# Optimization experiments

Hardware: AMD Instinct MI355X
Metric: run time of the kernel (lower is better)

## Reference

```python
import jax, jax.numpy as jnp
import numpy as np
from jax import lax

K = 3
PAD = 1
K2 = K * K


def _conv(x, w, b):
    dn = lax.conv_dimension_numbers(x.shape, w.shape, ('NCHW', 'OIHW', 'NCHW'))
    y = lax.conv_general_dilated(x, w, (1, 1), [(PAD, PAD), (PAD, PAD)], dimension_numbers=dn)
    return y + b[None, :, None, None]


def _gather(x, iy, ix):
    # x: [B,C,H,W]; iy,ix: [B,K2,H,W] int32 -> [B,C,K2,H,W]
    B, C, H, W = x.shape
    flat = x.reshape(B, C, H * W)
    idx = iy * W + ix  # [B,K2,H,W]
    return jax.vmap(lambda xb, ib: xb[:, ib])(flat, idx)


def _deform_conv2d(x, offset_w, offset_b, mask_w, mask_b, weight):
    B, C, H, W = x.shape
    O = weight.shape[0]
    offset = _conv(x, offset_w, offset_b)            # [B,2*K2,H,W]
    mask = jax.nn.sigmoid(_conv(x, mask_w, mask_b))  # [B,K2,H,W]

    off = offset.reshape(B, K2, 2, H, W)
    oy, ox = off[:, :, 0], off[:, :, 1]              # [B,K2,H,W]

    ki = (jnp.arange(K2) // K).astype(x.dtype)       # kernel row per tap
    kj = (jnp.arange(K2) % K).astype(x.dtype)        # kernel col per tap
    base_y = (jnp.arange(H) - PAD).astype(x.dtype)
    base_x = (jnp.arange(W) - PAD).astype(x.dtype)

    py = oy + base_y[None, None, :, None] + ki[None, :, None, None]  # [B,K2,H,W]
    px = ox + base_x[None, None, None, :] + kj[None, :, None, None]

    y0 = jnp.floor(py)
    x0 = jnp.floor(px)
    dy = py - y0
    dx = px - x0
    y0i = y0.astype(jnp.int32)
    x0i = x0.astype(jnp.int32)

    acc = jnp.zeros((B, C, K2, H, W), dtype=x.dtype)
    for (yc, xc, wgt) in [
        (y0i,     x0i,     (1 - dy) * (1 - dx)),
        (y0i,     x0i + 1, (1 - dy) * dx),
        (y0i + 1, x0i,     dy * (1 - dx)),
        (y0i + 1, x0i + 1, dy * dx),
    ]:
        valid = ((yc >= 0) & (yc < H) & (xc >= 0) & (xc < W)).astype(x.dtype)
        g = _gather(x, jnp.clip(yc, 0, H - 1), jnp.clip(xc, 0, W - 1))  # [B,C,K2,H,W]
        acc = acc + g * (wgt * valid)[:, None]

    modulated = acc * mask[:, None]                  # [B,C,K2,H,W]
    w2 = weight.reshape(O, C, K2)
    return jnp.einsum('bckhw,ock->bohw', modulated, w2)


def setup_inputs() -> dict:
    key = jax.random.key(0)
    ks = jax.random.split(key, 6)
    B, C, O, H, W = 4, 64, 64, 128, 128
    return {
        'x': jax.random.normal(ks[0], (B, C, H, W), jnp.float32),
        'offset_w': jax.random.normal(ks[1], (2 * K2, C, K, K), jnp.float32) * 0.05,
        'offset_b': jax.random.normal(ks[2], (2 * K2,), jnp.float32) * 0.05,
        'mask_w': jax.random.normal(ks[3], (K2, C, K, K), jnp.float32) * 0.05,
        'mask_b': jnp.full((K2,), 0.5, jnp.float32),
        'weight': jax.random.normal(ks[5], (O, C, K, K), jnp.float32) * (1.0 / np.sqrt(C * K2)),
    }


def reference(x, offset_w, offset_b, mask_w, mask_b, weight):
    return _deform_conv2d(x, offset_w, offset_b, mask_w, mask_b, weight)
```

## Files before the change

kernel.cpp:

```cpp
#include <hip/hip_runtime.h>
#include <math.h>

#define BB 4
#define CC 64
#define OO 64
#define HH 128
#define WW 128
#define HWsz (HH * WW)

typedef __attribute__((ext_vector_type(8))) _Float16 half8;
typedef __attribute__((ext_vector_type(4))) float floatx4;

__global__ __launch_bounds__(256) void pre_kernel(
    const float* __restrict__ x, const float* __restrict__ wgt,
    const float* __restrict__ ow, const float* __restrict__ mw,
    _Float16* __restrict__ xh, _Float16* __restrict__ waf,
    _Float16* __restrict__ wcf)
{
    int bid = blockIdx.x;
    int tid = threadIdx.x;
    if (bid < 512) {
        int b = bid >> 7, y = bid & 127;
        int px = tid & 127;
        int ch = (tid >> 7) * 32;
        const float* xp = x + (size_t)(b * CC + ch) * HWsz + y * WW + px;
        _Float16 buf[32];
#pragma unroll
        for (int q = 0; q < 32; ++q)
            buf[q] = (_Float16)xp[(size_t)q * HWsz];
        _Float16* dst = xh + ((size_t)(b * HH + y) * WW + px) * 64 + ch;
#pragma unroll
        for (int q = 0; q < 4; ++q)
            *(half8*)&dst[q * 8] = *(const half8*)&buf[q * 8];
    } else {
        int i = (bid - 512) * 256 + tid;
        if (i < 36864) {
            int j = i & 7, lane = (i >> 3) & 63, rest = i >> 9;
            int m = rest & 3, kh = (rest >> 2) & 1, k = rest >> 3;
            int o = m * 16 + (lane & 15);
            int c = kh * 32 + ((lane >> 4) << 3) + j;
            waf[i] = (_Float16)wgt[o * 576 + c * 9 + k];
        } else if (i < 55296) {
            int t = i - 36864;
            int j = t & 7, lane = (t >> 3) & 63, rest = t >> 9;
            int m = rest & 1, kh = (rest >> 1) & 1, k = rest >> 2;
            int o = m * 16 + (lane & 15);
            int c = kh * 32 + ((lane >> 4) << 3) + j;
            float v = 0.f;
            if (o < 18) v = ow[o * 576 + c * 9 + k];
            else if (o < 27) v = mw[(o - 18) * 576 + c * 9 + k];
            wcf[t] = (_Float16)v;
        }
    }
}

__global__ __launch_bounds__(1024, 1) void fused_kernel(
    const _Float16* __restrict__ xh, const _Float16* __restrict__ waf,
    const _Float16* __restrict__ wcf, const float* __restrict__ ob,
    const float* __restrict__ mb, float* __restrict__ out)
{
    __shared__ __align__(16) _Float16 lds_waf[36864];
    __shared__ _Float16 omh[16 * 27 * 16];
    __shared__ __align__(16) _Float16 blendb[16 * 2048];

    int tid = threadIdx.x;
    int gid = blockIdx.x;
    int sid = (gid & 7) * 32 + (gid >> 3);
    int b = sid >> 6;
    int t = sid & 63;
    int rq = t >> 1;
    int q = t & 1;

    int wv = tid >> 6;
    int lane = tid & 63;
    int s = wv & 3;
    int h = rq * 4 + (wv >> 2);
    int p0 = q << 6;
    int g = lane >> 4;
    int pl = lane & 15;
    int goff = g * 8;
    int xw = p0 + s * 16 + pl;
    int oct = lane & 7;
    int pxg = lane >> 3;

    const _Float16* xhb = xh + ((size_t)b << 20);
    _Float16* omw = &omh[wv * 27 * 16];
    _Float16* bbw = &blendb[wv * 2048];

    half8 stg[9];
    if (wv < 8) {
#pragma unroll
        for (int i = 0; i < 9; ++i)
            stg[i] = *(const half8*)(waf + ((wv * 9 + i) << 9) + lane * 8);
    }

    floatx4 accC0 = {0.f, 0.f, 0.f, 0.f};
    floatx4 accC1 = {0.f, 0.f, 0.f, 0.f};

#define CADDR(K, P, V) do {                                                  \
    int ky = (K) / 3, kx = (K) - ky * 3;                                     \
    int yy = h + ky - 1, xx = xw + kx - 1;                                   \
    V = (yy >= 0) & (yy < HH) & (xx >= 0) & (xx < WW);                       \
    int yc = min(max(yy, 0), HH - 1), xc = min(max(xx, 0), WW - 1);          \
    P = ((yc * WW + xc) << 6) + goff;                                        \
} while (0)

#define CONVTAP(K, S0, S1, V) do {                                           \
    const _Float16* wp = wcf + ((K) << 11) + lane * 8;                       \
    half8 w00 = *(const half8*)(wp + (0 << 9));                              \
    half8 w01 = *(const half8*)(wp + (1 << 9));                              \
    half8 w10 = *(const half8*)(wp + (2 << 9));                              \
    half8 w11 = *(const half8*)(wp + (3 << 9));                              \
    half8 z = {0, 0, 0, 0, 0, 0, 0, 0};                                     \
    half8 a0 = (V) ? S0 : z;                                                 \
    half8 a1 = (V) ? S1 : z;                                                 \
    accC0 = __builtin_amdgcn_mfma_f32_16x16x32_f16(w00, a0, accC0, 0, 0, 0); \
    accC1 = __builtin_amdgcn_mfma_f32_16x16x32_f16(w01, a0, accC1, 0, 0, 0); \
    accC0 = __builtin_amdgcn_mfma_f32_16x16x32_f16(w10, a1, accC0, 0, 0, 0); \
    accC1 = __builtin_amdgcn_mfma_f32_16x16x32_f16(w11, a1, accC1, 0, 0, 0); \
} while (0)

    {
        bool vA, vB;
        int pa, pb;
        half8 A0, A1, B0, B1;
        CADDR(0, pa, vA);
        A0 = *(const half8*)(xhb + pa);
        A1 = *(const half8*)(xhb + pa + 32);
#pragma unroll 1
        for (int kp = 0; kp < 4; ++kp) {
            int k = kp * 2;
            CADDR(k + 1, pb, vB);
            B0 = *(const half8*)(xhb + pb);
            B1 = *(const half8*)(xhb + pb + 32);
            CONVTAP(k, A0, A1, vA);
            CADDR(k + 2, pa, vA);
            A0 = *(const half8*)(xhb + pa);
            A1 = *(const half8*)(xhb + pa + 32);
            CONVTAP(k + 1, B0, B1, vB);
        }
        CONVTAP(8, A0, A1, vA);
    }

#pragma unroll
    for (int j = 0; j < 4; ++j) {
        int o = g * 4 + j;
        omw[o * 16 + pl] = (_Float16)(accC0[j] + ob[o]);
        int o2 = 16 + g * 4 + j;
        float v = accC1[j];
        if (o2 < 18) omw[o2 * 16 + pl] = (_Float16)(v + ob[o2]);
        else if (o2 < 27)
            omw[o2 * 16 + pl] =
                (_Float16)(1.0f / (1.0f + expf(-(v + mb[o2 - 18]))));
    }

    if (wv < 8) {
#pragma unroll
        for (int i = 0; i < 9; ++i)
            *(half8*)&lds_waf[((wv * 9 + i) << 9) + lane * 8] = stg[i];
    }
    __syncthreads();

    floatx4 acc0 = {0.f, 0.f, 0.f, 0.f}, acc1 = {0.f, 0.f, 0.f, 0.f};
    floatx4 acc2 = {0.f, 0.f, 0.f, 0.f}, acc3 = {0.f, 0.f, 0.f, 0.f};

#define MKT(K, P, U00, U01, U10, U11, I00, I01, I10, I11) do {               \
    int ky = (K) / 3, kx = (K) - ky * 3;                                     \
    float oy = (float)omw[(2 * (K)) * 16 + (P)];                             \
    float ox = (float)omw[(2 * (K) + 1) * 16 + (P)];                         \
    float mk = (float)omw[(18 + (K)) * 16 + (P)];                            \
    float py = oy + (float)(h + ky - 1);                                     \
    float qx = ox + (float)(p0 + s * 16 + (P) + kx - 1);                     \
    float y0f = floorf(py), x0f = floorf(qx);                                \
    float dyy = py - y0f, dxx = qx - x0f;                                    \
    int y0 = (int)y0f, x0 = (int)x0f;                                        \
    int y1 = y0 + 1, x1 = x0 + 1;                                            \
    bool vy0 = (y0 >= 0) & (y0 < HH), vy1 = (y1 >= 0) & (y1 < HH);           \
    bool vx0 = (x0 >= 0) & (x0 < WW), vx1 = (x1 >= 0) & (x1 < WW);           \
    U00 = (vy0 & vx0) ? (1.f - dyy) * (1.f - dxx) * mk : 0.f;                \
    U01 = (vy0 & vx1) ? (1.f - dyy) * dxx * mk : 0.f;                        \
    U10 = (vy1 & vx0) ? dyy * (1.f - dxx) * mk : 0.f;                        \
    U11 = (vy1 & vx1) ? dyy * dxx * mk : 0.f;                                \
    int yc0 = min(max(y0, 0), HH - 1), yc1 = min(max(y1, 0), HH - 1);        \
    int xc0 = min(max(x0, 0), WW - 1), xc1 = min(max(x1, 0), WW - 1);        \
    I00 = ((yc0 * WW + xc0) << 6) + oct * 8;                                 \
    I01 = ((yc0 * WW + xc1) << 6) + oct * 8;                                 \
    I10 = ((yc1 * WW + xc0) << 6) + oct * 8;                                 \
    I11 = ((yc1 * WW + xc1) << 6) + oct * 8;                                 \
} while (0)

#define SPLAT8(H) ((half8){(H), (H), (H), (H), (H), (H), (H), (H)})
#define MF(Q, B, A) A = __builtin_amdgcn_mfma_f32_16x16x32_f16(Q, B, A, 0, 0, 0)

#define DECLG(S)                                                             \
    float u0##S, u1##S, u2##S, u3##S, u4##S, u5##S, u6##S, u7##S;            \
    half8 r0##S, r1##S, r2##S, r3##S, r4##S, r5##S, r6##S, r7##S;

#define GLOAD(K, S) do {                                                     \
    int i0, i1, i2, i3, i4, i5, i6, i7;                                      \
    MKT(K, pxg, u0##S, u1##S, u2##S, u3##S, i0, i1, i2, i3);                 \
    MKT(K, 8 + pxg, u4##S, u5##S, u6##S, u7##S, i4, i5, i6, i7);             \
    r0##S = *(const half8*)(xhb + i0);                                       \
    r1##S = *(const half8*)(xhb + i1);                                       \
    r2##S = *(const half8*)(xhb + i2);                                       \
    r3##S = *(const half8*)(xhb + i3);                                       \
    r4##S = *(const half8*)(xhb + i4);                                       \
    r5##S = *(const half8*)(xhb + i5);                                       \
    r6##S = *(const half8*)(xhb + i6);                                       \
    r7##S = *(const half8*)(xhb + i7);                                       \
} while (0)

#define BW(K, S) do {                                                        \
    half8 bfA = r0##S * SPLAT8((_Float16)u0##S);                             \
    bfA = bfA + r1##S * SPLAT8((_Float16)u1##S);                             \
    bfA = bfA + r2##S * SPLAT8((_Float16)u2##S);                             \
    bfA = bfA + r3##S * SPLAT8((_Float16)u3##S);                             \
    half8 bfB = r4##S * SPLAT8((_Float16)u4##S);                             \
    bfB = bfB + r5##S * SPLAT8((_Float16)u5##S);                             \
    bfB = bfB + r6##S * SPLAT8((_Float16)u6##S);                             \
    bfB = bfB + r7##S * SPLAT8((_Float16)u7##S);                             \
    _Float16* bb = bbw + (((K) & 1) << 10);                                  \
    *(half8*)&bb[(pxg << 6) + ((oct ^ pxg) << 3)] = bfA;                     \
    *(half8*)&bb[((8 + pxg) << 6) + ((oct ^ pxg) << 3)] = bfB;               \
} while (0)

#define CONS(K) do {                                                         \
    const _Float16* bbr = bbw + (((K) & 1) << 10);                           \
    half8 bf = *(const half8*)&bbr[(pl << 6) + ((g ^ (pl & 7)) << 3)];       \
    half8 bd = *(const half8*)&bbr[(pl << 6) + (((g + 4) ^ (pl & 7)) << 3)]; \
    const _Float16* wk = &lds_waf[((K) << 12) + lane * 8];                   \
    half8 q0 = *(const half8*)(wk + (0 << 9));                               \
    half8 q1 = *(const half8*)(wk + (1 << 9));                               \
    half8 q2 = *(const half8*)(wk + (2 << 9));                               \
    half8 q3 = *(const half8*)(wk + (3 << 9));                               \
    half8 q4 = *(const half8*)(wk + (4 << 9));                               \
    half8 q5 = *(const half8*)(wk + (5 << 9));                               \
    half8 q6 = *(const half8*)(wk + (6 << 9));                               \
    half8 q7 = *(const half8*)(wk + (7 << 9));                               \
    MF(q0, bf, acc0); MF(q1, bf, acc1); MF(q2, bf, acc2); MF(q3, bf, acc3);  \
    MF(q4, bd, acc0); MF(q5, bd, acc1); MF(q6, bd, acc2); MF(q7, bd, acc3);  \
} while (0)

#define ITER(K, S) do {                                                      \
    const _Float16* bbr = bbw + (((K) & 1) << 10);                           \
    half8 bf = *(const half8*)&bbr[(pl << 6) + ((g ^ (pl & 7)) << 3)];       \
    half8 bd = *(const half8*)&bbr[(pl << 6) + (((g + 4) ^ (pl & 7)) << 3)]; \
    GLOAD((K) + 1, S);                                                       \
    const _Float16* wk = &lds_waf[((K) << 12) + lane * 8];                   \
    half8 q0 = *(const half8*)(wk + (0 << 9));                               \
    half8 q1 = *(const half8*)(wk + (1 << 9));                               \
    half8 q2 = *(const half8*)(wk + (2 << 9));                               \
    half8 q3 = *(const half8*)(wk + (3 << 9));                               \
    half8 q4 = *(const half8*)(wk + (4 << 9));                               \
    half8 q5 = *(const half8*)(wk + (5 << 9));                               \
    half8 q6 = *(const half8*)(wk + (6 << 9));                               \
    half8 q7 = *(const half8*)(wk + (7 << 9));                               \
    MF(q0, bf, acc0); MF(q1, bf, acc1); MF(q2, bf, acc2); MF(q3, bf, acc3);  \
    MF(q4, bd, acc0); MF(q5, bd, acc1); MF(q6, bd, acc2); MF(q7, bd, acc3);  \
    BW((K) + 1, S);                                                          \
} while (0)

    {
        DECLG(A)
        DECLG(B)
        GLOAD(0, A);
        BW(0, A);
        ITER(0, B);
        ITER(1, A);
        ITER(2, B);
        ITER(3, A);
        ITER(4, B);
        ITER(5, A);
        ITER(6, B);
        ITER(7, A);
        CONS(8);
    }

    float* outp = out + (size_t)b * OO * HWsz + h * WW + p0 + s * 16 + pl;
#pragma unroll
    for (int j = 0; j < 4; ++j) outp[(size_t)(g * 4 + j) * HWsz] = acc0[j];
#pragma unroll
    for (int j = 0; j < 4; ++j) outp[(size_t)(16 + g * 4 + j) * HWsz] = acc1[j];
#pragma unroll
    for (int j = 0; j < 4; ++j) outp[(size_t)(32 + g * 4 + j) * HWsz] = acc2[j];
#pragma unroll
    for (int j = 0; j < 4; ++j) outp[(size_t)(48 + g * 4 + j) * HWsz] = acc3[j];
}

extern "C" void kernel_launch(void* const* d_in, const int* in_sizes, int n_in,
                              void* d_out, int out_size, void* d_ws, size_t ws_size,
                              hipStream_t stream)
{
    const float* x   = (const float*)d_in[0];
    const float* ow  = (const float*)d_in[1];
    const float* ob  = (const float*)d_in[2];
    const float* mw  = (const float*)d_in[3];
    const float* mb  = (const float*)d_in[4];
    const float* wgt = (const float*)d_in[5];
    float* out = (float*)d_out;

    _Float16* xh  = (_Float16*)d_ws;
    _Float16* waf = xh + (size_t)BB * HWsz * 64;
    _Float16* wcf = waf + 36864;

    pre_kernel<<<dim3(512 + 216), dim3(256), 0, stream>>>(
        x, wgt, ow, mw, xh, waf, wcf);
    fused_kernel<<<dim3(256), dim3(1024), 0, stream>>>(
        xh, waf, wcf, ob, mb, out);
}
```

Before: 44.33 us.

## Stage input halo window in LDS for offset conv; read main weights from global

Each block now cooperatively loads a 6x68 halo window of the fp16 channels-last input into swizzled LDS, and the offset/mask conv taps read from it instead of doing per-wave global loads with bounds checks. To free LDS for the window, the 72KB main-weight staging is removed and the deformable-conv MFMA loop reads its weight fragments directly from global memory (L1/L2 cached). This trades redundant global input reads for an extra barrier and global weight loads in the hot inner loop.

```diff
diff --git a/kernel.cpp b/kernel.cpp
--- a/kernel.cpp
+++ b/kernel.cpp
@@ -59,7 +59,7 @@
     const _Float16* __restrict__ wcf, const float* __restrict__ ob,
     const float* __restrict__ mb, float* __restrict__ out)
 {
-    __shared__ __align__(16) _Float16 lds_waf[36864];
+    __shared__ __align__(16) _Float16 win[6 * 68 * 64];
     __shared__ _Float16 omh[16 * 27 * 16];
     __shared__ __align__(16) _Float16 blendb[16 * 2048];
 
@@ -78,69 +78,58 @@
     int p0 = q << 6;
     int g = lane >> 4;
     int pl = lane & 15;
-    int goff = g * 8;
-    int xw = p0 + s * 16 + pl;
     int oct = lane & 7;
     int pxg = lane >> 3;
+    int h0 = rq * 4;
 
     const _Float16* xhb = xh + ((size_t)b << 20);
     _Float16* omw = &omh[wv * 27 * 16];
     _Float16* bbw = &blendb[wv * 2048];
 
-    half8 stg[9];
-    if (wv < 8) {
-#pragma unroll
-        for (int i = 0; i < 9; ++i)
-            stg[i] = *(const half8*)(waf + ((wv * 9 + i) << 9) + lane * 8);
-    }
+    {
+        half8 z = {0, 0, 0, 0, 0, 0, 0, 0};
+#pragma unroll
+        for (int it = 0; it < 4; ++it) {
+            int ch = tid + it * 1024;
+            if (ch < 3264) {
+                int o8 = ch & 7;
+                int rc = ch >> 3;
+                int r = rc / 68;
+                int cc = rc - r * 68;
+                int gy = h0 - 1 + r;
+                int gx = p0 - 1 + cc;
+                half8 v = z;
+                if ((cc < 66) & (gy >= 0) & (gy < HH) & (gx >= 0) & (gx < WW))
+                    v = *(const half8*)(xhb + (((size_t)gy * WW + gx) << 6) + o8 * 8);
+                *(half8*)&win[((r * 68 + cc) << 6) + ((o8 ^ (cc & 7)) << 3)] = v;
+            }
+        }
+    }
+    __syncthreads();
 
     floatx4 accC0 = {0.f, 0.f, 0.f, 0.f};
     floatx4 accC1 = {0.f, 0.f, 0.f, 0.f};
 
-#define CADDR(K, P, V) do {                                                  \
+#define CONVTAP(K) do {                                                      \
     int ky = (K) / 3, kx = (K) - ky * 3;                                     \
-    int yy = h + ky - 1, xx = xw + kx - 1;                                   \
-    V = (yy >= 0) & (yy < HH) & (xx >= 0) & (xx < WW);                       \
-    int yc = min(max(yy, 0), HH - 1), xc = min(max(xx, 0), WW - 1);          \
-    P = ((yc * WW + xc) << 6) + goff;                                        \
-} while (0)
-
-#define CONVTAP(K, S0, S1, V) do {                                           \
+    int r = (wv >> 2) + ky;                                                  \
+    int c = s * 16 + pl + kx;                                                \
+    const _Float16* wb = &win[((r * 68 + c) << 6)];                          \
+    half8 a0 = *(const half8*)&wb[((g ^ (c & 7)) << 3)];                     \
+    half8 a1 = *(const half8*)&wb[(((g + 4) ^ (c & 7)) << 3)];               \
     const _Float16* wp = wcf + ((K) << 11) + lane * 8;                       \
     half8 w00 = *(const half8*)(wp + (0 << 9));                              \
     half8 w01 = *(const half8*)(wp + (1 << 9));                              \
     half8 w10 = *(const half8*)(wp + (2 << 9));                              \
     half8 w11 = *(const half8*)(wp + (3 << 9));                              \
-    half8 z = {0, 0, 0, 0, 0, 0, 0, 0};                                     \
-    half8 a0 = (V) ? S0 : z;                                                 \
-    half8 a1 = (V) ? S1 : z;                                                 \
     accC0 = __builtin_amdgcn_mfma_f32_16x16x32_f16(w00, a0, accC0, 0, 0, 0); \
     accC1 = __builtin_amdgcn_mfma_f32_16x16x32_f16(w01, a0, accC1, 0, 0, 0); \
     accC0 = __builtin_amdgcn_mfma_f32_16x16x32_f16(w10, a1, accC0, 0, 0, 0); \
     accC1 = __builtin_amdgcn_mfma_f32_16x16x32_f16(w11, a1, accC1, 0, 0, 0); \
 } while (0)
 
-    {
-        bool vA, vB;
-        int pa, pb;
-        half8 A0, A1, B0, B1;
-        CADDR(0, pa, vA);
-        A0 = *(const half8*)(xhb + pa);
-        A1 = *(const half8*)(xhb + pa + 32);
-#pragma unroll 1
-        for (int kp = 0; kp < 4; ++kp) {
-            int k = kp * 2;
-            CADDR(k + 1, pb, vB);
-            B0 = *(const half8*)(xhb + pb);
-            B1 = *(const half8*)(xhb + pb + 32);
-            CONVTAP(k, A0, A1, vA);
-            CADDR(k + 2, pa, vA);
-            A0 = *(const half8*)(xhb + pa);
-            A1 = *(const half8*)(xhb + pa + 32);
-            CONVTAP(k + 1, B0, B1, vB);
-        }
-        CONVTAP(8, A0, A1, vA);
-    }
+    CONVTAP(0); CONVTAP(1); CONVTAP(2); CONVTAP(3); CONVTAP(4);
+    CONVTAP(5); CONVTAP(6); CONVTAP(7); CONVTAP(8);
 
 #pragma unroll
     for (int j = 0; j < 4; ++j) {
@@ -153,13 +142,6 @@
             omw[o2 * 16 + pl] =
                 (_Float16)(1.0f / (1.0f + expf(-(v + mb[o2 - 18]))));
     }
-
-    if (wv < 8) {
-#pragma unroll
-        for (int i = 0; i < 9; ++i)
-            *(half8*)&lds_waf[((wv * 9 + i) << 9) + lane * 8] = stg[i];
-    }
-    __syncthreads();
 
     floatx4 acc0 = {0.f, 0.f, 0.f, 0.f}, acc1 = {0.f, 0.f, 0.f, 0.f};
     floatx4 acc2 = {0.f, 0.f, 0.f, 0.f}, acc3 = {0.f, 0.f, 0.f, 0.f};
@@ -228,7 +210,7 @@
     const _Float16* bbr = bbw + (((K) & 1) << 10);                           \
     half8 bf = *(const half8*)&bbr[(pl << 6) + ((g ^ (pl & 7)) << 3)];       \
     half8 bd = *(const half8*)&bbr[(pl << 6) + (((g + 4) ^ (pl & 7)) << 3)]; \
-    const _Float16* wk = &lds_waf[((K) << 12) + lane * 8];                   \
+    const _Float16* wk = waf + ((K) << 12) + lane * 8;                       \
     half8 q0 = *(const half8*)(wk + (0 << 9));                               \
     half8 q1 = *(const half8*)(wk + (1 << 9));                               \
     half8 q2 = *(const half8*)(wk + (2 << 9));                               \
@@ -246,7 +228,7 @@
     half8 bf = *(const half8*)&bbr[(pl << 6) + ((g ^ (pl & 7)) << 3)];       \
     half8 bd = *(const half8*)&bbr[(pl << 6) + (((g + 4) ^ (pl & 7)) << 3)]; \
     GLOAD((K) + 1, S);                                                       \
-    const _Float16* wk = &lds_waf[((K) << 12) + lane * 8];                   \
+    const _Float16* wk = waf + ((K) << 12) + lane * 8;                       \
     half8 q0 = *(const half8*)(wk + (0 << 9));                               \
     half8 q1 = *(const half8*)(wk + (1 << 9));                               \
     half8 q2 = *(const half8*)(wk + (2 << 9));                               \
```

New measurement: 48.01 us. 8.3% more time.
